# Performance work log

Hardware: AMD Instinct MI355X
Metric: run time of the kernel (lower is better)

Reference implementation:

```python
import jax, jax.numpy as jnp
import numpy as np

COMMITMENT_COST = 0.25
N_EMBED = 1024
EMB_DIM = 256

def setup_inputs() -> dict:
    key = jax.random.key(0)
    k1, k2 = jax.random.split(key)
    z = jax.random.normal(k1, (32, EMB_DIM, 32, 32), dtype=jnp.float32)
    # embedding.weight.data.uniform_(-1/n_embed, 1/n_embed)
    embedding = jax.random.uniform(k2, (N_EMBED, EMB_DIM), dtype=jnp.float32,
                                   minval=-1.0 / N_EMBED, maxval=1.0 / N_EMBED)
    return {"z": z, "embedding": embedding}

def reference(z, embedding):
    # NCHW -> NHWC
    zp = jnp.transpose(z, (0, 2, 3, 1))            # [B,H,W,D]
    in_shape = zp.shape
    flat = zp.reshape(-1, in_shape[-1])            # [N,D]
    # squared L2 distances (argmin equivalent to p=2 cdist argmin)
    d2 = (jnp.sum(flat * flat, axis=1, keepdims=True)
          - 2.0 * (flat @ embedding.T)
          + jnp.sum(embedding * embedding, axis=1))  # [N,K]
    idx = jnp.argmin(d2, axis=1)                   # [N]
    # one-hot @ codebook == direct gather
    z_quant = embedding[idx].reshape(in_shape)     # [B,H,W,D]
    codebook_loss = jnp.mean((z_quant - jax.lax.stop_gradient(zp)) ** 2)
    commitment_loss = jnp.mean((zp - jax.lax.stop_gradient(z_quant)) ** 2)
    loss = codebook_loss + COMMITMENT_COST * commitment_loss
    # straight-through estimator
    z_st = zp + jax.lax.stop_gradient(z_quant - zp)
    z_st = jnp.transpose(z_st, (0, 3, 1, 2))       # NHWC -> NCHW
    return (z_st, loss, codebook_loss, commitment_loss)
```

## Files before the change

### kernel.cpp

```cpp
#include <hip/hip_runtime.h>
#include <hip/hip_bf16.h>
#include <stdint.h>


typedef short v8s __attribute__((ext_vector_type(8)));
typedef float v4f __attribute__((ext_vector_type(4)));

__device__ inline unsigned short f2bf(float f) {
    uint32_t u = __float_as_uint(f);
    return (unsigned short)((u + 0x7fffu + ((u >> 16) & 1u)) >> 16);
}

__global__ __launch_bounds__(512) void k_prep_a(const float* __restrict__ z,
                                                unsigned short* __restrict__ Abf,
                                                float* __restrict__ rowN2) {
    __shared__ float P[64][33];
    int tid = threadIdx.x;
    int b = blockIdx.x >> 4, hw0 = (blockIdx.x & 15) << 6;
    int t15 = tid & 15, dblk = tid >> 4;
    const float* zp = z + ((size_t)b << 18) + (size_t)(dblk << 3) * 1024 + hw0 + (t15 << 2);
    float4 L[8];
#pragma unroll
    for (int j = 0; j < 8; j++)
        L[j] = *(const float4*)(zp + (size_t)j * 1024);
    const float* Lf = (const float*)L;
    v8s* Aout = (v8s*)Abf + ((size_t)(b * 1024 + hw0 + (t15 << 2))) * 32 + dblk;
#pragma unroll
    for (int c = 0; c < 4; c++) {
        union { v8s v; unsigned short s[8]; } u;
        float p = 0.f;
#pragma unroll
        for (int j = 0; j < 8; j++) {
            float v = Lf[j * 4 + c];
            u.s[j] = f2bf(v);
            p += v * v;
        }
        Aout[(size_t)c * 32] = u.v;
        P[(t15 << 2) + c][dblk] = p;
    }
    __syncthreads();
    if (tid < 64) {
        float s = 0.f;
#pragma unroll
        for (int k = 0; k < 32; k++) s += P[tid][k];
        rowN2[b * 1024 + hw0 + tid] = s;
    }
}

__global__ __launch_bounds__(256) void k_prep_e(const float* __restrict__ E,
                                                v8s* __restrict__ Esw,
                                                float* __restrict__ nE,
                                                float* __restrict__ accum) {
    __shared__ float Ef[16][264];
    int q = blockIdx.x, tid = threadIdx.x;
    const float4* Ein = (const float4*)(E + ((size_t)q << 12));
#pragma unroll
    for (int i = 0; i < 4; i++) {
        int f4 = i * 256 + tid;
        int row = f4 >> 6, c4 = (f4 & 63) << 2;
        *(float4*)&Ef[row][c4] = Ein[f4];
    }
    __syncthreads();
    {
        int c = tid >> 4, l = tid & 15;
        float s = 0.f;
#pragma unroll
        for (int j = 0; j < 16; j++) { float v = Ef[c][l + 16 * j]; s += v * v; }
#pragma unroll
        for (int off = 1; off < 16; off <<= 1) s += __shfl_xor(s, off);
        if (l == 0) nE[q * 16 + c] = 0.5f * s;
    }
#pragma unroll
    for (int i = 0; i < 2; i++) {
        int u = tid + i * 256;
        int um = u & 15, ug = (u >> 4) & 3, udc = (u >> 6) & 7;
        int d0 = udc * 32 + ug * 8;
        union { v8s v; unsigned short s[8]; } pk;
#pragma unroll
        for (int e = 0; e < 8; e++) pk.s[e] = f2bf(Ef[um][d0 + e]);
        Esw[((size_t)q << 9) + u] = pk.v;
    }
    if (q == 0 && tid == 0) accum[0] = 0.f;
}

__global__ __launch_bounds__(256, 2) void k_main(
        const unsigned short* __restrict__ Abf,
        const v8s* __restrict__ Esw,
        const float* __restrict__ nE,
        unsigned long long* __restrict__ cand) {
    __shared__ v8s B[2][2048];
    __shared__ float nEl[256];

    int tid = threadIdx.x;
    int lane = tid & 63, w = tid >> 6;
    int g = lane >> 4, m = lane & 15;
    int cs = blockIdx.x & 3;
    int R0 = (blockIdx.x >> 2) << 8;
    int C0 = cs << 8;

    nEl[tid] = nE[C0 + tid];

    v8s a[4][8];
    {
        const v8s* Ap = (const v8s*)Abf;
#pragma unroll
        for (int s = 0; s < 4; s++) {
            int row = R0 + (w << 6) + (s << 4) + m;
#pragma unroll
            for (int dc = 0; dc < 8; dc++)
                a[s][dc] = Ap[(size_t)row * 32 + dc * 4 + g];
        }
    }

#define STAGE(ch, buf)                                                        \
    {                                                                         \
        _Pragma("unroll")                                                     \
        for (int j = 0; j < 8; j++) {                                         \
            __builtin_amdgcn_global_load_lds(                                 \
                (const __attribute__((address_space(1))) void*)               \
                    (Esw + ((size_t)(C0 + (ch) * 64) << 5) + (j << 8)         \
                         + (w << 6) + lane),                                  \
                (__attribute__((address_space(3))) void*)                     \
                    &B[buf][(j << 8) + (w << 6)],                             \
                16, 0, 0);                                                    \
        }                                                                     \
    }

    float best[4][4]; int bidx[4][4];
#pragma unroll
    for (int s = 0; s < 4; s++)
#pragma unroll
        for (int r = 0; r < 4; r++) { best[s][r] = 3.4e38f; bidx[s][r] = 0; }

    STAGE(0, 0);
#pragma unroll 1
    for (int ct = 0; ct < 4; ct++) {
        int cur = ct & 1;
        __syncthreads();
        if (ct < 3) STAGE(ct + 1, cur ^ 1);
#pragma unroll
        for (int t = 0; t < 4; t++) {
            float ne = nEl[(ct << 6) + (t << 4) + m];
            v4f acc[4];
#pragma unroll
            for (int s = 0; s < 4; s++) acc[s] = (v4f){0.f, 0.f, 0.f, 0.f};
#pragma unroll
            for (int dc = 0; dc < 8; dc++) {
                v8s bf = B[cur][(t << 9) + (dc << 6) + (g << 4) + m];
                acc[0] = __builtin_amdgcn_mfma_f32_16x16x32_bf16(a[0][dc], bf, acc[0], 0, 0, 0);
                acc[1] = __builtin_amdgcn_mfma_f32_16x16x32_bf16(a[1][dc], bf, acc[1], 0, 0, 0);
                acc[2] = __builtin_amdgcn_mfma_f32_16x16x32_bf16(a[2][dc], bf, acc[2], 0, 0, 0);
                acc[3] = __builtin_amdgcn_mfma_f32_16x16x32_bf16(a[3][dc], bf, acc[3], 0, 0, 0);
            }
            int code = C0 + (ct << 6) + (t << 4) + m;
#pragma unroll
            for (int s = 0; s < 4; s++)
#pragma unroll
                for (int r = 0; r < 4; r++) {
                    float sc = ne - acc[s][r];
                    if (sc < best[s][r]) { best[s][r] = sc; bidx[s][r] = code; }
                }
        }
    }

#pragma unroll
    for (int s = 0; s < 4; s++)
#pragma unroll
        for (int r = 0; r < 4; r++) {
            uint32_t sb = __float_as_uint(best[s][r]);
            sb = (sb & 0x80000000u) ? ~sb : (sb | 0x80000000u);
            unsigned long long pk = ((unsigned long long)sb << 32) | (uint32_t)bidx[s][r];
#pragma unroll
            for (int off = 1; off < 16; off <<= 1) {
                unsigned long long o = __shfl_xor(pk, off);
                if (o < pk) pk = o;
            }
            if (m == 0)
                cand[((size_t)cs << 15) + R0 + (w << 6) + (s << 4) + (g << 2) + r] = pk;
        }
#undef STAGE
}

__global__ __launch_bounds__(256) void k_out(const float* __restrict__ E,
                                             const unsigned long long* __restrict__ cand,
                                             const float* __restrict__ rowN2,
                                             float* __restrict__ out,
                                             float* __restrict__ accum) {
    __shared__ float4 Eg4[2048];
    __shared__ int    kk[32];
    __shared__ float  ss[32];
    int bid = blockIdx.x;
    int b = bid >> 5, hw0 = (bid & 31) << 5;
    int tid = threadIdx.x;
    int lane = tid & 63, w = tid >> 6;
    if (tid < 32) {
        int n = b * 1024 + hw0 + tid;
        unsigned long long bv = cand[n];
#pragma unroll
        for (int s = 1; s < 4; s++) {
            unsigned long long v = cand[((size_t)s << 15) + n];
            if (v < bv) bv = v;
        }
        kk[tid] = (int)(bv & 0xffffffffu);
        uint32_t sb = (uint32_t)(bv >> 32);
        uint32_t u = (sb & 0x80000000u) ? (sb & 0x7fffffffu) : ~sb;
        ss[tid] = rowN2[n] + 2.0f * __uint_as_float(u);
    }
    __syncthreads();
    if (w == 0) {
        float v = (lane < 32) ? ss[lane] : 0.f;
#pragma unroll
        for (int off = 1; off < 64; off <<= 1) v += __shfl_xor(v, off);
        if (lane == 0) atomicAdd(accum, v);
    }
#pragma unroll
    for (int i = 0; i < 8; i++) {
        int row = w + (i << 2);
        int k = kk[row];
        float4 v = ((const float4*)(E + ((size_t)k << 8)))[lane];
        Eg4[(row << 6) + (lane ^ row)] = v;
    }
    __syncthreads();
    float* ob = out + ((size_t)b << 18);
    int hwl = tid & 31, dq0 = tid >> 5;
    int hwp = hw0 + hwl;
#pragma unroll
    for (int i = 0; i < 8; i++) {
        int dq = dq0 + (i << 3);
        float4 ev = Eg4[(hwl << 6) + (dq ^ hwl)];
        size_t o = ((size_t)dq << 12) + hwp;
        ob[o] = ev.x; ob[o + 1024] = ev.y; ob[o + 2048] = ev.z; ob[o + 3072] = ev.w;
    }
}

__global__ void k_loss(const float* __restrict__ accum, float* __restrict__ out) {
    if (threadIdx.x == 0) {
        float s = accum[0] * (1.0f / 8388608.0f);
        out[8388608] = 1.25f * s;
        out[8388609] = s;
        out[8388610] = s;
    }
}

extern "C" void kernel_launch(void* const* d_in, const int* in_sizes, int n_in,
                              void* d_out, int out_size, void* d_ws, size_t ws_size,
                              hipStream_t stream) {
    const float* z = (const float*)d_in[0];
    const float* E = (const float*)d_in[1];
    char* ws = (char*)d_ws;
    unsigned short*     Abf   = (unsigned short*)(ws);
    v8s*                Esw   = (v8s*)(ws + 16777216);
    float*              nE    = (float*)(ws + 17301504);
    unsigned long long* cand  = (unsigned long long*)(ws + 17305600);
    float*              rowN2 = (float*)(ws + 18354176);
    float*              accum = (float*)(ws + 18485248);
    float* out = (float*)d_out;

    hipLaunchKernelGGL(k_prep_e, dim3(64),   dim3(256), 0, stream, E, Esw, nE, accum);
    hipLaunchKernelGGL(k_prep_a, dim3(512),  dim3(512), 0, stream, z, Abf, rowN2);
    hipLaunchKernelGGL(k_main,   dim3(512),  dim3(256), 0, stream, Abf, Esw, nE, cand);
    hipLaunchKernelGGL(k_out,    dim3(1024), dim3(256), 0, stream, E, cand, rowN2, out, accum);
    hipLaunchKernelGGL(k_loss,   dim3(1),    dim3(64),  0, stream, accum, out);
}
```

Measured before the change: 136.4 us.

## Fuse z transpose and bf16 conversion into main distance kernel

Removes the separate k_prep_a pass, which wrote a bf16 transposed copy of z plus row norms. k_main now reads fp32 z directly in NCHW layout, converts it to bf16 fragments in registers, and computes row norms with shuffles. Only the cs==0 blocks write those norms. The block index mapping changes so the four column-split blocks sharing the same rows are 128 blocks apart, and the first codebook stage is issued before the A load so the two overlap. This drops one launch and a 16MB intermediate round trip. In exchange, each z row is read by four blocks with scalar strided loads (coalesced across m only), where before it was one vectorised pass.

```diff
diff --git a/kernel.cpp b/kernel.cpp
--- a/kernel.cpp
+++ b/kernel.cpp
@@ -9,42 +9,6 @@
 __device__ inline unsigned short f2bf(float f) {
     uint32_t u = __float_as_uint(f);
     return (unsigned short)((u + 0x7fffu + ((u >> 16) & 1u)) >> 16);
-}
-
-__global__ __launch_bounds__(512) void k_prep_a(const float* __restrict__ z,
-                                                unsigned short* __restrict__ Abf,
-                                                float* __restrict__ rowN2) {
-    __shared__ float P[64][33];
-    int tid = threadIdx.x;
-    int b = blockIdx.x >> 4, hw0 = (blockIdx.x & 15) << 6;
-    int t15 = tid & 15, dblk = tid >> 4;
-    const float* zp = z + ((size_t)b << 18) + (size_t)(dblk << 3) * 1024 + hw0 + (t15 << 2);
-    float4 L[8];
-#pragma unroll
-    for (int j = 0; j < 8; j++)
-        L[j] = *(const float4*)(zp + (size_t)j * 1024);
-    const float* Lf = (const float*)L;
-    v8s* Aout = (v8s*)Abf + ((size_t)(b * 1024 + hw0 + (t15 << 2))) * 32 + dblk;
-#pragma unroll
-    for (int c = 0; c < 4; c++) {
-        union { v8s v; unsigned short s[8]; } u;
-        float p = 0.f;
-#pragma unroll
-        for (int j = 0; j < 8; j++) {
-            float v = Lf[j * 4 + c];
-            u.s[j] = f2bf(v);
-            p += v * v;
-        }
-        Aout[(size_t)c * 32] = u.v;
-        P[(t15 << 2) + c][dblk] = p;
-    }
-    __syncthreads();
-    if (tid < 64) {
-        float s = 0.f;
-#pragma unroll
-        for (int k = 0; k < 32; k++) s += P[tid][k];
-        rowN2[b * 1024 + hw0 + tid] = s;
-    }
 }
 
 __global__ __launch_bounds__(256) void k_prep_e(const float* __restrict__ E,
@@ -84,33 +48,24 @@
 }
 
 __global__ __launch_bounds__(256, 2) void k_main(
-        const unsigned short* __restrict__ Abf,
+        const float* __restrict__ z,
         const v8s* __restrict__ Esw,
         const float* __restrict__ nE,
-        unsigned long long* __restrict__ cand) {
+        unsigned long long* __restrict__ cand,
+        float* __restrict__ rowN2) {
     __shared__ v8s B[2][2048];
     __shared__ float nEl[256];
 
     int tid = threadIdx.x;
     int lane = tid & 63, w = tid >> 6;
     int g = lane >> 4, m = lane & 15;
-    int cs = blockIdx.x & 3;
-    int R0 = (blockIdx.x >> 2) << 8;
+    int cs = blockIdx.x >> 7;
+    int rg = blockIdx.x & 127;
+    int R0 = rg << 8;
     int C0 = cs << 8;
+    int b = rg >> 2, hw0 = (rg & 3) << 8;
 
     nEl[tid] = nE[C0 + tid];
-
-    v8s a[4][8];
-    {
-        const v8s* Ap = (const v8s*)Abf;
-#pragma unroll
-        for (int s = 0; s < 4; s++) {
-            int row = R0 + (w << 6) + (s << 4) + m;
-#pragma unroll
-            for (int dc = 0; dc < 8; dc++)
-                a[s][dc] = Ap[(size_t)row * 32 + dc * 4 + g];
-        }
-    }
 
 #define STAGE(ch, buf)                                                        \
     {                                                                         \
@@ -126,13 +81,39 @@
         }                                                                     \
     }
 
+    STAGE(0, 0);
+
+    v8s a[4][8];
+    {
+        const float* zb = z + ((size_t)b << 18) + hw0 + (w << 6) + m;
+#pragma unroll
+        for (int s = 0; s < 4; s++) {
+            const float* zr = zb + (s << 4) + ((size_t)g << 13);
+            float p = 0.f;
+#pragma unroll
+            for (int dc = 0; dc < 8; dc++) {
+                union { v8s v; unsigned short h[8]; } u;
+#pragma unroll
+                for (int j = 0; j < 8; j++) {
+                    float v = zr[((size_t)(dc << 5) + j) << 10];
+                    u.h[j] = f2bf(v);
+                    p += v * v;
+                }
+                a[s][dc] = u.v;
+            }
+            p += __shfl_xor(p, 16);
+            p += __shfl_xor(p, 32);
+            if (cs == 0 && g == 0)
+                rowN2[R0 + (w << 6) + (s << 4) + m] = p;
+        }
+    }
+
     float best[4][4]; int bidx[4][4];
 #pragma unroll
     for (int s = 0; s < 4; s++)
 #pragma unroll
         for (int r = 0; r < 4; r++) { best[s][r] = 3.4e38f; bidx[s][r] = 0; }
 
-    STAGE(0, 0);
 #pragma unroll 1
     for (int ct = 0; ct < 4; ct++) {
         int cur = ct & 1;
@@ -248,17 +229,15 @@
     const float* z = (const float*)d_in[0];
     const float* E = (const float*)d_in[1];
     char* ws = (char*)d_ws;
-    unsigned short*     Abf   = (unsigned short*)(ws);
-    v8s*                Esw   = (v8s*)(ws + 16777216);
-    float*              nE    = (float*)(ws + 17301504);
-    unsigned long long* cand  = (unsigned long long*)(ws + 17305600);
-    float*              rowN2 = (float*)(ws + 18354176);
-    float*              accum = (float*)(ws + 18485248);
+    v8s*                Esw   = (v8s*)(ws);
+    float*              nE    = (float*)(ws + 524288);
+    unsigned long long* cand  = (unsigned long long*)(ws + 528384);
+    float*              rowN2 = (float*)(ws + 1576960);
+    float*              accum = (float*)(ws + 1708032);
     float* out = (float*)d_out;
 
     hipLaunchKernelGGL(k_prep_e, dim3(64),   dim3(256), 0, stream, E, Esw, nE, accum);
-    hipLaunchKernelGGL(k_prep_a, dim3(512),  dim3(512), 0, stream, z, Abf, rowN2);
-    hipLaunchKernelGGL(k_main,   dim3(512),  dim3(256), 0, stream, Abf, Esw, nE, cand);
+    hipLaunchKernelGGL(k_main,   dim3(512),  dim3(256), 0, stream, z, Esw, nE, cand, rowN2);
     hipLaunchKernelGGL(k_out,    dim3(1024), dim3(256), 0, stream, E, cand, rowN2, out, accum);
     hipLaunchKernelGGL(k_loss,   dim3(1),    dim3(64),  0, stream, accum, out);
 }
```

After: 148.7 us. 9.0% more time.
